# Kernel optimization log

Measured on AMD Instinct MI355X. Metric: run time of the kernel, lower is better.

Reference implementation:

```python
import jax, jax.numpy as jnp
import numpy as np

MAX_LOGIT = 30.0
COV_WEIGHT = 1.0


def setup_inputs() -> dict:
    key = jax.random.key(0)
    ks = jax.random.split(key, 8)
    B, T, S, H = 8, 100, 400, 256
    sc = 1.0 / np.sqrt(H)
    return {
        "decoder_outputs": jax.random.normal(ks[0], (B, T, H), jnp.float32),
        "encoder_outputs": jax.random.normal(ks[1], (B, S, H), jnp.float32),
        "src_mask": jnp.zeros((B, S), dtype=bool),
        "W_h": jax.random.normal(ks[2], (H, H), jnp.float32) * sc,
        "W_s": jax.random.normal(ks[3], (H, H), jnp.float32) * sc,
        "w_c": jax.random.normal(ks[4], (H,), jnp.float32) * sc,  # Linear(1,H) weight
        "v": jax.random.normal(ks[5], (H,), jnp.float32) * sc,    # Linear(H,1) weight
        "b_attn": jnp.zeros((H,), jnp.float32),
    }


def reference(decoder_outputs, encoder_outputs, src_mask, W_h, W_s, w_c, v, b_attn):
    B, T, H = decoder_outputs.shape
    S = encoder_outputs.shape[1]
    neg_inf = jnp.float32(-jnp.inf)

    Wh = jnp.einsum('bsh,hk->bsk', encoder_outputs, W_h)   # [B,S,H]
    Ws = jnp.einsum('bth,hk->btk', decoder_outputs, W_s)   # [B,T,H]
    # E_base: [B,T,S,H]
    E_base = Wh[:, None, :, :] + Ws[:, :, None, :] + b_attn

    def logits(x):
        e = jnp.einsum('btsh,h->bts', jnp.tanh(x), v)
        e = jnp.clip(e, -MAX_LOGIT, MAX_LOGIT)
        return jnp.where(src_mask[:, None, :], neg_inf, e)

    A_prelim = jax.nn.softmax(logits(E_base), axis=-1)      # [B,T,S]
    cum = jnp.cumsum(A_prelim, axis=1)
    cov_shifted = jnp.concatenate(
        [jnp.zeros((B, 1, S), A_prelim.dtype), cum[:, :-1, :]], axis=1)  # [B,T,S]

    # W_c applied to scalar coverage: outer product with w_c -> [B,T,S,H]
    E_final = logits(E_base + cov_shifted[..., None] * w_c)
    A_final = jax.nn.softmax(E_final, axis=-1)              # [B,T,S]

    context = jnp.einsum('bts,bsh->bth', A_final, encoder_outputs)
    cov_loss = (COV_WEIGHT * jnp.sum(jnp.minimum(A_final, cov_shifted), axis=-1).mean())[None]
    return context, A_final, cov_loss
```

## Files before the change

kernel.cpp:

```cpp
#include <hip/hip_runtime.h>
#include <math.h>

#define B_ 8
#define T_ 100
#define S_ 400
#define H_ 256
#define BT_ (B_ * T_)
#define MAXL 30.0f

#define AF_OFF (BT_ * H_)
#define LOSS_OFF (BT_ * H_ + BT_ * S_)

#define WH_OFF 0
#define WS_OFF (B_ * S_ * H_)
#define ACOV_OFF (WS_OFF + BT_ * H_)

__device__ __forceinline__ float fast_tanh(float x) {
    float e = __expf(2.0f * x);
    return 1.0f - 2.0f * __builtin_amdgcn_rcpf(e + 1.0f);
}

__device__ __forceinline__ float wave_sum(float p) {
#pragma unroll
    for (int off = 32; off; off >>= 1) p += __shfl_xor(p, off, 64);
    return p;
}

__device__ __forceinline__ float wave_max(float p) {
#pragma unroll
    for (int off = 32; off; off >>= 1) p = fmaxf(p, __shfl_xor(p, off, 64));
    return p;
}

__device__ __forceinline__ float group16_sum(float p) {
    p += __shfl_xor(p, 1, 64);
    p += __shfl_xor(p, 2, 64);
    p += __shfl_xor(p, 4, 64);
    p += __shfl_xor(p, 8, 64);
    return p;
}

__device__ __forceinline__ float tanh_dot4(float4 wv, float4 bse, float4 vv) {
    return fast_tanh(wv.x + bse.x) * vv.x + fast_tanh(wv.y + bse.y) * vv.y +
           fast_tanh(wv.z + bse.z) * vv.z + fast_tanh(wv.w + bse.w) * vv.w;
}
__device__ __forceinline__ float tanh_dot4c(float4 wv, float4 bse, float c,
                                            float4 wc, float4 vv) {
    return fast_tanh(wv.x + bse.x + c * wc.x) * vv.x +
           fast_tanh(wv.y + bse.y + c * wc.y) * vv.y +
           fast_tanh(wv.z + bse.z + c * wc.z) * vv.z +
           fast_tanh(wv.w + bse.w + c * wc.w) * vv.w;
}

#define ROWS 4
__global__ __launch_bounds__(256) void k_gemm(
    const float* __restrict__ dec, const float* __restrict__ enc,
    const float* __restrict__ W_h, const float* __restrict__ W_s,
    const float* __restrict__ b_attn,
    float* __restrict__ Wh, float* __restrict__ Ws) {
    const int tid = threadIdx.x;
    const int blk = blockIdx.x;
    const int NB_ENC = (B_ * S_) / ROWS;

    const float* in;
    const float* W;
    float* out;
    int r0;
    float bias = 0.f;
    if (blk < NB_ENC) {
        in = enc; W = W_h; out = Wh; r0 = blk * ROWS;
    } else {
        in = dec; W = W_s; out = Ws; r0 = (blk - NB_ENC) * ROWS;
        bias = b_attn[tid];
    }

    const float* i0 = in + (size_t)r0 * H_;
    const float* i1 = i0 + H_;
    const float* i2 = i1 + H_;
    const float* i3 = i2 + H_;
    const float* Wp = W + tid;

    float a0 = bias, a1 = bias, a2 = bias, a3 = bias;
#pragma unroll 8
    for (int h = 0; h < H_; ++h) {
        float w = Wp[(size_t)h * H_];
        a0 = fmaf(i0[h], w, a0);
        a1 = fmaf(i1[h], w, a1);
        a2 = fmaf(i2[h], w, a2);
        a3 = fmaf(i3[h], w, a3);
    }
    out[(size_t)(r0 + 0) * H_ + tid] = a0;
    out[(size_t)(r0 + 1) * H_ + tid] = a1;
    out[(size_t)(r0 + 2) * H_ + tid] = a2;
    out[(size_t)(r0 + 3) * H_ + tid] = a3;
}

__global__ __launch_bounds__(512, 3) void k_prelim(
    const float* __restrict__ Wh, const float* __restrict__ Ws,
    const float* __restrict__ v,
    const unsigned char* __restrict__ mask,
    float* __restrict__ A) {
    __shared__ float e_lds[S_];
    __shared__ float red[16];
    const int blk = blockIdx.x;
    const int b = blk & 7;
    const int t = blk >> 3;
    const int bt = b * T_ + t;
    const int tid = threadIdx.x;
    const int lane = tid & 63;
    const int wid = tid >> 6;
    const int l = tid & 15;
    const int g = tid >> 4;

    const float4* WsP = reinterpret_cast<const float4*>(Ws + (size_t)bt * H_ + l * 16);
    const float4* vP = reinterpret_cast<const float4*>(v + l * 16);
    const float4 b0 = WsP[0], b1 = WsP[1], b2 = WsP[2], b3 = WsP[3];
    const float4 v0 = vP[0], v1 = vP[1], v2 = vP[2], v3 = vP[3];

    const float* WhB = Wh + (size_t)b * S_ * H_;
    const unsigned char* mb = mask + (size_t)b * S_;

    for (int s = g; s < S_; s += 32) {
        const float4* wp = reinterpret_cast<const float4*>(WhB + (size_t)s * H_ + l * 16);
        float4 w0 = wp[0], w1 = wp[1], w2 = wp[2], w3 = wp[3];
        float p = tanh_dot4(w0, b0, v0) + tanh_dot4(w1, b1, v1) +
                  tanh_dot4(w2, b2, v2) + tanh_dot4(w3, b3, v3);
        p = group16_sum(p);
        if (l == 0) {
            float e = fminf(fmaxf(p, -MAXL), MAXL);
            if (mb[s]) e = -INFINITY;
            e_lds[s] = e;
        }
    }
    __syncthreads();

    float mx = (tid < S_) ? e_lds[tid] : -INFINITY;
    mx = wave_max(mx);
    if (lane == 0) red[wid] = mx;
    __syncthreads();
    mx = fmaxf(fmaxf(fmaxf(red[0], red[1]), fmaxf(red[2], red[3])),
               fmaxf(fmaxf(red[4], red[5]), fmaxf(red[6], red[7])));

    float p = (tid < S_) ? __expf(e_lds[tid] - mx) : 0.f;
    float sum = wave_sum(p);
    if (lane == 0) red[8 + wid] = sum;
    __syncthreads();
    sum = ((red[8] + red[9]) + (red[10] + red[11])) +
          ((red[12] + red[13]) + (red[14] + red[15]));
    const float inv = __builtin_amdgcn_rcpf(sum);

    if (tid < S_) A[(size_t)bt * S_ + tid] = p * inv;
}

__global__ __launch_bounds__(256) void k_cumsum(float* __restrict__ A,
                                                float* __restrict__ out) {
    const int idx = blockIdx.x * 256 + threadIdx.x;
    if (idx == 0) out[LOSS_OFF] = 0.f;
    if (idx >= B_ * S_) return;
    const int b = idx / S_;
    const int s = idx - b * S_;
    float* col = A + (size_t)b * T_ * S_ + s;
    float run = 0.f;
#pragma unroll 10
    for (int t = 0; t < T_; ++t) {
        float a = col[(size_t)t * S_];
        col[(size_t)t * S_] = run;
        run += a;
    }
}

__global__ __launch_bounds__(512, 3) void k_final(
    const float* __restrict__ Wh, const float* __restrict__ Ws,
    const float* __restrict__ v,
    const float* __restrict__ w_c, const float* __restrict__ cov,
    const unsigned char* __restrict__ mask,
    const float* __restrict__ enc,
    float* __restrict__ out) {
    __shared__ float e_lds[S_];
    __shared__ float cov_lds[S_];
    __shared__ float ctx_part[H_];
    __shared__ float red[16];
    const int blk = blockIdx.x;
    const int b = blk & 7;
    const int t = blk >> 3;
    const int bt = b * T_ + t;
    const int tid = threadIdx.x;
    const int lane = tid & 63;
    const int wid = tid >> 6;
    const int l = tid & 15;
    const int g = tid >> 4;

    const float4* WsP = reinterpret_cast<const float4*>(Ws + (size_t)bt * H_ + l * 16);
    const float4* vP = reinterpret_cast<const float4*>(v + l * 16);
    const float4* wcP = reinterpret_cast<const float4*>(w_c + l * 16);
    const float4 b0 = WsP[0], b1 = WsP[1], b2 = WsP[2], b3 = WsP[3];
    const float4 v0 = vP[0], v1 = vP[1], v2 = vP[2], v3 = vP[3];
    const float4 c0 = wcP[0], c1 = wcP[1], c2 = wcP[2], c3 = wcP[3];

    float covreg = 0.f;
    if (tid < S_) {
        covreg = cov[(size_t)bt * S_ + tid];
        cov_lds[tid] = covreg;
    }
    __syncthreads();

    const float* WhB = Wh + (size_t)b * S_ * H_;
    const unsigned char* mb = mask + (size_t)b * S_;

    for (int s = g; s < S_; s += 32) {
        const float c = cov_lds[s];
        const float4* wp = reinterpret_cast<const float4*>(WhB + (size_t)s * H_ + l * 16);
        float4 w0 = wp[0], w1 = wp[1], w2 = wp[2], w3 = wp[3];
        float p = tanh_dot4c(w0, b0, c, c0, v0) + tanh_dot4c(w1, b1, c, c1, v1) +
                  tanh_dot4c(w2, b2, c, c2, v2) + tanh_dot4c(w3, b3, c, c3, v3);
        p = group16_sum(p);
        if (l == 0) {
            float e = fminf(fmaxf(p, -MAXL), MAXL);
            if (mb[s]) e = -INFINITY;
            e_lds[s] = e;
        }
    }
    __syncthreads();

    float mx = (tid < S_) ? e_lds[tid] : -INFINITY;
    mx = wave_max(mx);
    if (lane == 0) red[wid] = mx;
    __syncthreads();
    mx = fmaxf(fmaxf(fmaxf(red[0], red[1]), fmaxf(red[2], red[3])),
               fmaxf(fmaxf(red[4], red[5]), fmaxf(red[6], red[7])));

    float p = (tid < S_) ? __expf(e_lds[tid] - mx) : 0.f;
    float sum = wave_sum(p);
    if (lane == 0) red[8 + wid] = sum;
    __syncthreads();
    sum = ((red[8] + red[9]) + (red[10] + red[11])) +
          ((red[12] + red[13]) + (red[14] + red[15]));
    const float inv = __builtin_amdgcn_rcpf(sum);

    const float a = (tid < S_) ? p * inv : 0.f;

    float lp = (tid < S_) ? fminf(a, covreg) : 0.f;
    lp = wave_sum(lp);
    if (lane == 0) red[wid] = lp;

    if (tid < S_) {
        e_lds[tid] = a;
        out[AF_OFF + (size_t)bt * S_ + tid] = a;
    }
    __syncthreads();

    if (tid == 0) {
        float tot = ((red[0] + red[1]) + (red[2] + red[3])) +
                    ((red[4] + red[5]) + (red[6] + red[7]));
        atomicAdd(out + LOSS_OFF, tot * (1.0f / (B_ * T_)));
    }

    const int h = tid & (H_ - 1);
    const int half = tid >> 8;
    const int s0 = half * (S_ / 2);
    const float* eb = enc + ((size_t)b * S_ + s0) * H_ + h;
    float cacc = 0.f;
#pragma unroll 8
    for (int j = 0; j < S_ / 2; ++j) cacc += e_lds[s0 + j] * eb[(size_t)j * H_];
    if (half == 0) ctx_part[h] = cacc;
    __syncthreads();
    if (half == 1) out[(size_t)bt * H_ + h] = ctx_part[h] + cacc;
}

extern "C" void kernel_launch(void* const* d_in, const int* in_sizes, int n_in,
                              void* d_out, int out_size, void* d_ws, size_t ws_size,
                              hipStream_t stream) {
    const float* dec = (const float*)d_in[0];
    const float* enc = (const float*)d_in[1];
    const unsigned char* mask = (const unsigned char*)d_in[2];
    const float* W_h = (const float*)d_in[3];
    const float* W_s = (const float*)d_in[4];
    const float* w_c = (const float*)d_in[5];
    const float* v = (const float*)d_in[6];
    const float* b_attn = (const float*)d_in[7];

    float* out = (float*)d_out;
    float* ws = (float*)d_ws;
    float* Wh = ws + WH_OFF;
    float* Ws = ws + WS_OFF;
    float* Acov = ws + ACOV_OFF;

    const int nb_gemm = (B_ * S_) / ROWS + BT_ / ROWS;
    k_gemm<<<nb_gemm, 256, 0, stream>>>(dec, enc, W_h, W_s, b_attn, Wh, Ws);
    k_prelim<<<BT_, 512, 0, stream>>>(Wh, Ws, v, mask, Acov);
    k_cumsum<<<(B_ * S_ + 255) / 256, 256, 0, stream>>>(Acov, out);
    k_final<<<BT_, 512, 0, stream>>>(Wh, Ws, v, w_c, Acov, mask, enc, out);
}
```

Baseline: 179.7 us.

## Transpose Wh, prescale by 2/ln2, use one-thread-per-source tanh dot

The GEMM now writes Wh transposed ([B,H,S]) and pre-multiplies both projections by 2*log2(e). The attention kernels can then compute tanh via exp2 and rcp, and fold the sum(v) constant out of the dot product. Each thread now owns one source position and loops over H, reading coalesced columns. This removes the 16-lane shuffle reductions and the LDS staging of the logits. Other changes: k_cumsum uses smaller blocks, the launch_bounds occupancy hints are dropped, and the context accumulation is split across four independent FMA chains. The cost is a strided transposed store in the GEMM and per-thread loops over 256 elements, which may raise register pressure.

Result: faster. 163.8 us (-8.8%).

```diff
diff --git a/kernel.cpp b/kernel.cpp
--- a/kernel.cpp
+++ b/kernel.cpp
@@ -7,18 +7,14 @@
 #define H_ 256
 #define BT_ (B_ * T_)
 #define MAXL 30.0f
+#define K_EXP 2.885390081777927f
 
 #define AF_OFF (BT_ * H_)
 #define LOSS_OFF (BT_ * H_ + BT_ * S_)
 
-#define WH_OFF 0
-#define WS_OFF (B_ * S_ * H_)
-#define ACOV_OFF (WS_OFF + BT_ * H_)
-
-__device__ __forceinline__ float fast_tanh(float x) {
-    float e = __expf(2.0f * x);
-    return 1.0f - 2.0f * __builtin_amdgcn_rcpf(e + 1.0f);
-}
+#define WHT_OFF 0
+#define WSB_OFF (B_ * H_ * S_)
+#define ACOV_OFF (WSB_OFF + BT_ * H_)
 
 __device__ __forceinline__ float wave_sum(float p) {
 #pragma unroll
@@ -30,26 +26,6 @@
 #pragma unroll
     for (int off = 32; off; off >>= 1) p = fmaxf(p, __shfl_xor(p, off, 64));
     return p;
-}
-
-__device__ __forceinline__ float group16_sum(float p) {
-    p += __shfl_xor(p, 1, 64);
-    p += __shfl_xor(p, 2, 64);
-    p += __shfl_xor(p, 4, 64);
-    p += __shfl_xor(p, 8, 64);
-    return p;
-}
-
-__device__ __forceinline__ float tanh_dot4(float4 wv, float4 bse, float4 vv) {
-    return fast_tanh(wv.x + bse.x) * vv.x + fast_tanh(wv.y + bse.y) * vv.y +
-           fast_tanh(wv.z + bse.z) * vv.z + fast_tanh(wv.w + bse.w) * vv.w;
-}
-__device__ __forceinline__ float tanh_dot4c(float4 wv, float4 bse, float c,
-                                            float4 wc, float4 vv) {
-    return fast_tanh(wv.x + bse.x + c * wc.x) * vv.x +
-           fast_tanh(wv.y + bse.y + c * wc.y) * vv.y +
-           fast_tanh(wv.z + bse.z + c * wc.z) * vv.z +
-           fast_tanh(wv.w + bse.w + c * wc.w) * vv.w;
 }
 
 #define ROWS 4
@@ -57,50 +33,56 @@
     const float* __restrict__ dec, const float* __restrict__ enc,
     const float* __restrict__ W_h, const float* __restrict__ W_s,
     const float* __restrict__ b_attn,
-    float* __restrict__ Wh, float* __restrict__ Ws) {
+    float* __restrict__ WhT, float* __restrict__ Wsb) {
     const int tid = threadIdx.x;
     const int blk = blockIdx.x;
     const int NB_ENC = (B_ * S_) / ROWS;
 
-    const float* in;
-    const float* W;
-    float* out;
-    int r0;
-    float bias = 0.f;
+    float a0 = 0.f, a1 = 0.f, a2 = 0.f, a3 = 0.f;
+
     if (blk < NB_ENC) {
-        in = enc; W = W_h; out = Wh; r0 = blk * ROWS;
+        const int r0 = blk * ROWS;
+        const int b = r0 / S_, s0 = r0 - b * S_;
+        const float* in = enc + (size_t)r0 * H_;
+        const float* Wp = W_h + tid;
+#pragma unroll 8
+        for (int h = 0; h < H_; ++h) {
+            float w = Wp[(size_t)h * H_];
+            a0 = fmaf(in[h], w, a0);
+            a1 = fmaf(in[H_ + h], w, a1);
+            a2 = fmaf(in[2 * H_ + h], w, a2);
+            a3 = fmaf(in[3 * H_ + h], w, a3);
+        }
+        float* o = WhT + ((size_t)b * H_ + tid) * S_ + s0;
+        o[0] = K_EXP * a0;
+        o[1] = K_EXP * a1;
+        o[2] = K_EXP * a2;
+        o[3] = K_EXP * a3;
     } else {
-        in = dec; W = W_s; out = Ws; r0 = (blk - NB_ENC) * ROWS;
-        bias = b_attn[tid];
-    }
-
-    const float* i0 = in + (size_t)r0 * H_;
-    const float* i1 = i0 + H_;
-    const float* i2 = i1 + H_;
-    const float* i3 = i2 + H_;
-    const float* Wp = W + tid;
-
-    float a0 = bias, a1 = bias, a2 = bias, a3 = bias;
-#pragma unroll 8
-    for (int h = 0; h < H_; ++h) {
-        float w = Wp[(size_t)h * H_];
-        a0 = fmaf(i0[h], w, a0);
-        a1 = fmaf(i1[h], w, a1);
-        a2 = fmaf(i2[h], w, a2);
-        a3 = fmaf(i3[h], w, a3);
-    }
-    out[(size_t)(r0 + 0) * H_ + tid] = a0;
-    out[(size_t)(r0 + 1) * H_ + tid] = a1;
-    out[(size_t)(r0 + 2) * H_ + tid] = a2;
-    out[(size_t)(r0 + 3) * H_ + tid] = a3;
-}
-
-__global__ __launch_bounds__(512, 3) void k_prelim(
-    const float* __restrict__ Wh, const float* __restrict__ Ws,
+        const int bt0 = (blk - NB_ENC) * ROWS;
+        const float* in = dec + (size_t)bt0 * H_;
+        const float* Wp = W_s + tid;
+        const float bias = b_attn[tid];
+#pragma unroll 8
+        for (int h = 0; h < H_; ++h) {
+            float w = Wp[(size_t)h * H_];
+            a0 = fmaf(in[h], w, a0);
+            a1 = fmaf(in[H_ + h], w, a1);
+            a2 = fmaf(in[2 * H_ + h], w, a2);
+            a3 = fmaf(in[3 * H_ + h], w, a3);
+        }
+        Wsb[(size_t)(bt0 + 0) * H_ + tid] = K_EXP * (a0 + bias);
+        Wsb[(size_t)(bt0 + 1) * H_ + tid] = K_EXP * (a1 + bias);
+        Wsb[(size_t)(bt0 + 2) * H_ + tid] = K_EXP * (a2 + bias);
+        Wsb[(size_t)(bt0 + 3) * H_ + tid] = K_EXP * (a3 + bias);
+    }
+}
+
+__global__ __launch_bounds__(512) void k_prelim(
+    const float* __restrict__ WhT, const float* __restrict__ Wsb,
     const float* __restrict__ v,
     const unsigned char* __restrict__ mask,
     float* __restrict__ A) {
-    __shared__ float e_lds[S_];
     __shared__ float red[16];
     const int blk = blockIdx.x;
     const int b = blk & 7;
@@ -109,39 +91,37 @@
     const int tid = threadIdx.x;
     const int lane = tid & 63;
     const int wid = tid >> 6;
-    const int l = tid & 15;
-    const int g = tid >> 4;
-
-    const float4* WsP = reinterpret_cast<const float4*>(Ws + (size_t)bt * H_ + l * 16);
-    const float4* vP = reinterpret_cast<const float4*>(v + l * 16);
-    const float4 b0 = WsP[0], b1 = WsP[1], b2 = WsP[2], b3 = WsP[3];
-    const float4 v0 = vP[0], v1 = vP[1], v2 = vP[2], v3 = vP[3];
-
-    const float* WhB = Wh + (size_t)b * S_ * H_;
-    const unsigned char* mb = mask + (size_t)b * S_;
-
-    for (int s = g; s < S_; s += 32) {
-        const float4* wp = reinterpret_cast<const float4*>(WhB + (size_t)s * H_ + l * 16);
-        float4 w0 = wp[0], w1 = wp[1], w2 = wp[2], w3 = wp[3];
-        float p = tanh_dot4(w0, b0, v0) + tanh_dot4(w1, b1, v1) +
-                  tanh_dot4(w2, b2, v2) + tanh_dot4(w3, b3, v3);
-        p = group16_sum(p);
-        if (l == 0) {
-            float e = fminf(fmaxf(p, -MAXL), MAXL);
-            if (mb[s]) e = -INFINITY;
-            e_lds[s] = e;
-        }
-    }
-    __syncthreads();
-
-    float mx = (tid < S_) ? e_lds[tid] : -INFINITY;
-    mx = wave_max(mx);
+    const int s = tid;
+    const bool act = (s < S_);
+
+    const float4 vv4 = *reinterpret_cast<const float4*>(v + 4 * lane);
+    const float sumv = wave_sum((vv4.x + vv4.y) + (vv4.z + vv4.w));
+
+    const float* Wsr = Wsb + (size_t)bt * H_;
+    float acc = 0.f;
+    if (act) {
+        const float* wcol = WhT + (size_t)b * H_ * S_ + s;
+#pragma unroll 8
+        for (int h = 0; h < H_; ++h) {
+            float w = wcol[(size_t)h * S_];
+            float r = __builtin_amdgcn_rcpf(__builtin_amdgcn_exp2f(w + Wsr[h]) + 1.0f);
+            acc = fmaf(r, v[h], acc);
+        }
+    }
+
+    float e = -INFINITY;
+    if (act) {
+        e = fminf(fmaxf(sumv - 2.f * acc, -MAXL), MAXL);
+        if (mask[(size_t)b * S_ + s]) e = -INFINITY;
+    }
+
+    float mx = wave_max(e);
     if (lane == 0) red[wid] = mx;
     __syncthreads();
     mx = fmaxf(fmaxf(fmaxf(red[0], red[1]), fmaxf(red[2], red[3])),
                fmaxf(fmaxf(red[4], red[5]), fmaxf(red[6], red[7])));
 
-    float p = (tid < S_) ? __expf(e_lds[tid] - mx) : 0.f;
+    float p = act ? __expf(e - mx) : 0.f;
     float sum = wave_sum(p);
     if (lane == 0) red[8 + wid] = sum;
     __syncthreads();
@@ -149,12 +129,12 @@
           ((red[12] + red[13]) + (red[14] + red[15]));
     const float inv = __builtin_amdgcn_rcpf(sum);
 
-    if (tid < S_) A[(size_t)bt * S_ + tid] = p * inv;
-}
-
-__global__ __launch_bounds__(256) void k_cumsum(float* __restrict__ A,
-                                                float* __restrict__ out) {
-    const int idx = blockIdx.x * 256 + threadIdx.x;
+    if (act) A[(size_t)bt * S_ + s] = p * inv;
+}
+
+__global__ __launch_bounds__(64) void k_cumsum(float* __restrict__ A,
+                                               float* __restrict__ out) {
+    const int idx = blockIdx.x * 64 + threadIdx.x;
     if (idx == 0) out[LOSS_OFF] = 0.f;
     if (idx >= B_ * S_) return;
     const int b = idx / S_;
@@ -169,15 +149,14 @@
     }
 }
 
-__global__ __launch_bounds__(512, 3) void k_final(
-    const float* __restrict__ Wh, const float* __restrict__ Ws,
-    const float* __restrict__ v,
-    const float* __restrict__ w_c, const float* __restrict__ cov,
+__global__ __launch_bounds__(512) void k_final(
+    const float* __restrict__ WhT, const float* __restrict__ Wsb,
+    const float* __restrict__ v, const float* __restrict__ w_c,
+    const float* __restrict__ cov,
     const unsigned char* __restrict__ mask,
     const float* __restrict__ enc,
     float* __restrict__ out) {
     __shared__ float e_lds[S_];
-    __shared__ float cov_lds[S_];
     __shared__ float ctx_part[H_];
     __shared__ float red[16];
     const int blk = blockIdx.x;
@@ -187,49 +166,42 @@
     const int tid = threadIdx.x;
     const int lane = tid & 63;
     const int wid = tid >> 6;
-    const int l = tid & 15;
-    const int g = tid >> 4;
-
-    const float4* WsP = reinterpret_cast<const float4*>(Ws + (size_t)bt * H_ + l * 16);
-    const float4* vP = reinterpret_cast<const float4*>(v + l * 16);
-    const float4* wcP = reinterpret_cast<const float4*>(w_c + l * 16);
-    const float4 b0 = WsP[0], b1 = WsP[1], b2 = WsP[2], b3 = WsP[3];
-    const float4 v0 = vP[0], v1 = vP[1], v2 = vP[2], v3 = vP[3];
-    const float4 c0 = wcP[0], c1 = wcP[1], c2 = wcP[2], c3 = wcP[3];
-
-    float covreg = 0.f;
-    if (tid < S_) {
-        covreg = cov[(size_t)bt * S_ + tid];
-        cov_lds[tid] = covreg;
-    }
-    __syncthreads();
-
-    const float* WhB = Wh + (size_t)b * S_ * H_;
-    const unsigned char* mb = mask + (size_t)b * S_;
-
-    for (int s = g; s < S_; s += 32) {
-        const float c = cov_lds[s];
-        const float4* wp = reinterpret_cast<const float4*>(WhB + (size_t)s * H_ + l * 16);
-        float4 w0 = wp[0], w1 = wp[1], w2 = wp[2], w3 = wp[3];
-        float p = tanh_dot4c(w0, b0, c, c0, v0) + tanh_dot4c(w1, b1, c, c1, v1) +
-                  tanh_dot4c(w2, b2, c, c2, v2) + tanh_dot4c(w3, b3, c, c3, v3);
-        p = group16_sum(p);
-        if (l == 0) {
-            float e = fminf(fmaxf(p, -MAXL), MAXL);
-            if (mb[s]) e = -INFINITY;
-            e_lds[s] = e;
-        }
-    }
-    __syncthreads();
-
-    float mx = (tid < S_) ? e_lds[tid] : -INFINITY;
-    mx = wave_max(mx);
+    const int s = tid;
+    const bool act = (s < S_);
+
+    const float4 vv4 = *reinterpret_cast<const float4*>(v + 4 * lane);
+    const float sumv = wave_sum((vv4.x + vv4.y) + (vv4.z + vv4.w));
+
+    float c = 0.f;
+    if (act) c = cov[(size_t)bt * S_ + s];
+    const float ck = K_EXP * c;
+
+    const float* Wsr = Wsb + (size_t)bt * H_;
+    float acc = 0.f;
+    if (act) {
+        const float* wcol = WhT + (size_t)b * H_ * S_ + s;
+#pragma unroll 8
+        for (int h = 0; h < H_; ++h) {
+            float w = wcol[(size_t)h * S_];
+            float arg = fmaf(ck, w_c[h], w + Wsr[h]);
+            float r = __builtin_amdgcn_rcpf(__builtin_amdgcn_exp2f(arg) + 1.0f);
+            acc = fmaf(r, v[h], acc);
+        }
+    }
+
+    float e = -INFINITY;
+    if (act) {
+        e = fminf(fmaxf(sumv - 2.f * acc, -MAXL), MAXL);
+        if (mask[(size_t)b * S_ + s]) e = -INFINITY;
+    }
+
+    float mx = wave_max(e);
     if (lane == 0) red[wid] = mx;
     __syncthreads();
     mx = fmaxf(fmaxf(fmaxf(red[0], red[1]), fmaxf(red[2], red[3])),
                fmaxf(fmaxf(red[4], red[5]), fmaxf(red[6], red[7])));
 
-    float p = (tid < S_) ? __expf(e_lds[tid] - mx) : 0.f;
+    float p = act ? __expf(e - mx) : 0.f;
     float sum = wave_sum(p);
     if (lane == 0) red[8 + wid] = sum;
     __syncthreads();
@@ -237,15 +209,15 @@
           ((red[12] + red[13]) + (red[14] + red[15]));
     const float inv = __builtin_amdgcn_rcpf(sum);
 
-    const float a = (tid < S_) ? p * inv : 0.f;
-
-    float lp = (tid < S_) ? fminf(a, covreg) : 0.f;
+    const float a = act ? p * inv : 0.f;
+
+    float lp = act ? fminf(a, c) : 0.f;
     lp = wave_sum(lp);
     if (lane == 0) red[wid] = lp;
 
-    if (tid < S_) {
-        e_lds[tid] = a;
-        out[AF_OFF + (size_t)bt * S_ + tid] = a;
+    if (act) {
+        e_lds[s] = a;
+        out[AF_OFF + (size_t)bt * S_ + s] = a;
     }
     __syncthreads();
 
@@ -259,12 +231,17 @@
     const int half = tid >> 8;
     const int s0 = half * (S_ / 2);
     const float* eb = enc + ((size_t)b * S_ + s0) * H_ + h;
-    float cacc = 0.f;
-#pragma unroll 8
-    for (int j = 0; j < S_ / 2; ++j) cacc += e_lds[s0 + j] * eb[(size_t)j * H_];
-    if (half == 0) ctx_part[h] = cacc;
-    __syncthreads();
-    if (half == 1) out[(size_t)bt * H_ + h] = ctx_part[h] + cacc;
+    float ca = 0.f, cb = 0.f, cc = 0.f, cd = 0.f;
+#pragma unroll 5
+    for (int j = 0; j < S_ / 2; j += 4) {
+        ca = fmaf(e_lds[s0 + j], eb[(size_t)j * H_], ca);
+        cb = fmaf(e_lds[s0 + j + 1], eb[(size_t)(j + 1) * H_], cb);
+        cc = fmaf(e_lds[s0 + j + 2], eb[(size_t)(j + 2) * H_], cc);
+        cd = fmaf(e_lds[s0 + j + 3], eb[(size_t)(j + 3) * H_], cd);
+    }
+    if (half == 0) ctx_part[h] = (ca + cb) + (cc + cd);
+    __syncthreads();
+    if (half == 1) out[(size_t)bt * H_ + h] = ctx_part[h] + (ca + cb) + (cc + cd);
 }
 
 extern "C" void kernel_launch(void* const* d_in, const int* in_sizes, int n_in,
@@ -281,13 +258,13 @@
 
     float* out = (float*)d_out;
     float* ws = (float*)d_ws;
-    float* Wh = ws + WH_OFF;
-    float* Ws = ws + WS_OFF;
+    float* WhT = ws + WHT_OFF;
+    float* Wsb = ws + WSB_OFF;
     float* Acov = ws + ACOV_OFF;
 
     const int nb_gemm = (B_ * S_) / ROWS + BT_ / ROWS;
-    k_gemm<<<nb_gemm, 256, 0, stream>>>(dec, enc, W_h, W_s, b_attn, Wh, Ws);
-    k_prelim<<<BT_, 512, 0, stream>>>(Wh, Ws, v, mask, Acov);
-    k_cumsum<<<(B_ * S_ + 255) / 256, 256, 0, stream>>>(Acov, out);
-    k_final<<<BT_, 512, 0, stream>>>(Wh, Ws, v, w_c, Acov, mask, enc, out);
-}
+    k_gemm<<<nb_gemm, 256, 0, stream>>>(dec, enc, W_h, W_s, b_attn, WhT, Wsb);
+    k_prelim<<<BT_, 512, 0, stream>>>(WhT, Wsb, v, mask, Acov);
+    k_cumsum<<<(B_ * S_ + 63) / 64, 64, 0, stream>>>(Acov, out);
+    k_final<<<BT_, 512, 0, stream>>>(WhT, Wsb, v, w_c, Acov, mask, enc, out);
+}
```
